# Kernel tuning notes

Measured on AMD Instinct MI355X. Metric: run time of the kernel, lower is better.

Reference implementation:

```python
import jax, jax.numpy as jnp
import numpy as np

H = 128  # hidden size
IN = 12  # input size
OUT = 4  # output classes


def _lstm_scan(gates_x, Whh, B, dtype, collect_ys):
    """gates_x: [T,B,4H] precomputed input-to-hidden gates (with biases).
    PyTorch gate order: i, f, g, o."""
    h0 = jnp.zeros((B, H), dtype)
    c0 = jnp.zeros((B, H), dtype)

    def step(carry, gx):
        h, c = carry
        g = gx + h @ Whh.T  # [B,4H]
        i, f, gg, o = jnp.split(g, 4, axis=-1)
        c = jax.nn.sigmoid(f) * c + jax.nn.sigmoid(i) * jnp.tanh(gg)
        h = jax.nn.sigmoid(o) * jnp.tanh(c)
        return (h, c), (h if collect_ys else None)

    (hT, cT), hs = jax.lax.scan(step, (h0, c0), gates_x)
    return hs, hT


def setup_inputs() -> dict:
    key = jax.random.key(0)
    ks = jax.random.split(key, 12)
    B, T = 256, 2048
    s = 1.0 / np.sqrt(H)  # torch LSTM/Linear init scale
    u = lambda k, shape: jax.random.uniform(k, shape, jnp.float32, -s, s)
    return {
        "x": jax.random.normal(ks[0], (B, T, IN), jnp.float32),
        "W_ih_l0": u(ks[1], (4 * H, IN)),
        "W_hh_l0": u(ks[2], (4 * H, H)),
        "b_ih_l0": u(ks[3], (4 * H,)),
        "b_hh_l0": u(ks[4], (4 * H,)),
        "W_ih_l1": u(ks[5], (4 * H, H)),
        "W_hh_l1": u(ks[6], (4 * H, H)),
        "b_ih_l1": u(ks[7], (4 * H,)),
        "b_hh_l1": u(ks[8], (4 * H,)),
        "W_out": u(ks[9], (OUT, H)),
        "b_out": u(ks[10], (OUT,)),
    }


def reference(x, W_ih_l0, W_hh_l0, b_ih_l0, b_hh_l0,
              W_ih_l1, W_hh_l1, b_ih_l1, b_hh_l1, W_out, b_out):
    B = x.shape[0]
    # layer 0: precompute all input projections at once -> [T,B,4H]
    gx0 = jnp.einsum('bti,gi->tbg', x, W_ih_l0) + b_ih_l0 + b_hh_l0
    hs0, _ = _lstm_scan(gx0, W_hh_l0, B, x.dtype, collect_ys=True)  # [T,B,H]
    # layer 1: only final hidden state is needed (r_out[:, -1] == h_T)
    gx1 = jnp.einsum('tbh,gh->tbg', hs0, W_ih_l1) + b_ih_l1 + b_hh_l1
    _, hT = _lstm_scan(gx1, W_hh_l1, B, x.dtype, collect_ys=False)  # [B,H]
    return hT @ W_out.T + b_out  # [B,4]
```

## Files before the change

### kernel.cpp

```cpp
#include <hip/hip_runtime.h>
#include <cstdint>
#include <cstddef>

#define H      128
#define IN_    12
#define GATES  512
#define B_     256
#define T_     2048
#define TCMAX  512
#define TT     64
#define PS     520

#define REP32(M) M(0) M(1) M(2) M(3) M(4) M(5) M(6) M(7) M(8) M(9) M(10) M(11) \
  M(12) M(13) M(14) M(15) M(16) M(17) M(18) M(19) M(20) M(21) M(22) M(23) \
  M(24) M(25) M(26) M(27) M(28) M(29) M(30) M(31)

__device__ __forceinline__ float sigmoidf_(float x) {
    return 1.f / (1.f + __expf(-x));
}
__device__ __forceinline__ float tanhf_(float x) {
    return 2.f / (1.f + __expf(-2.f * x)) - 1.f;
}
__device__ __forceinline__ float dot4f(float4 w, float4 h, float a) {
    return fmaf(w.x, h.x, fmaf(w.y, h.y, fmaf(w.z, h.z, fmaf(w.w, h.w, a))));
}

template<bool IS_L0>
__global__ __launch_bounds__(1024) void lstm_scan(
    const float* __restrict__ x_or_gx,
    const float* __restrict__ Wih,
    const float* __restrict__ Whh,
    const float* __restrict__ bih, const float* __restrict__ bhh,
    float* __restrict__ hs0,
    float* __restrict__ state,
    int tc, int chunk)
{
    const int b   = blockIdx.x;
    const int tid = threadIdx.x;
    const int ks  = tid >> 7;
    const int q   = tid & 127;

    extern __shared__ float smem[];
    float* sh_part = smem;
    float* sh_h    = smem + 8 * PS;
    float* sh_x    = sh_h + H;

#define LOADW(i) \
    const float4* wr##i = (const float4*)(Whh + (size_t)(4*q+i)*H + 16*ks); \
    float4 w##i##0 = wr##i[0], w##i##1 = wr##i[1], w##i##2 = wr##i[2], w##i##3 = wr##i[3];
    LOADW(0) LOADW(1) LOADW(2) LOADW(3)
#undef LOADW

    float4 wx0 = {0,0,0,0}, wx1 = {0,0,0,0}, wx2 = {0,0,0,0}, wx3 = {0,0,0,0};
    if constexpr (IS_L0) {
        if (ks >= 1 && ks <= 3) {
            wx0 = *(const float4*)(Wih + (size_t)(4*q+0)*IN_ + 4*(ks-1));
            wx1 = *(const float4*)(Wih + (size_t)(4*q+1)*IN_ + 4*(ks-1));
            wx2 = *(const float4*)(Wih + (size_t)(4*q+2)*IN_ + 4*(ks-1));
            wx3 = *(const float4*)(Wih + (size_t)(4*q+3)*IN_ + 4*(ks-1));
        }
        const float* xs = x_or_gx + ((size_t)b * T_ + (size_t)chunk * tc) * IN_;
        for (int i = tid; i < tc * IN_; i += 1024) sh_x[i] = xs[i];
    }

    float bias0 = 0, bias1 = 0, bias2 = 0, bias3 = 0;
    float cur0 = 0, cur1 = 0, cur2 = 0, cur3 = 0;
    float hreg = 0.f, creg = 0.f;
    const float* gxb = nullptr;
    if constexpr (!IS_L0) gxb = x_or_gx + (size_t)b * tc * GATES;

    if (tid < H) {
        if constexpr (IS_L0) {
            bias0 = bih[tid]       + bhh[tid];
            bias1 = bih[tid + 128] + bhh[tid + 128];
            bias2 = bih[tid + 256] + bhh[tid + 256];
            bias3 = bih[tid + 384] + bhh[tid + 384];
        } else {
            cur0 = gxb[tid]; cur1 = gxb[tid + 128];
            cur2 = gxb[tid + 256]; cur3 = gxb[tid + 384];
        }
        if (chunk) { hreg = state[b*2*H + tid]; creg = state[b*2*H + H + tid]; }
        sh_h[tid] = hreg;
    }
    __syncthreads();

    float* hs_out = nullptr;
    if constexpr (IS_L0) hs_out = hs0 + (size_t)b * tc * H;

    const float4* sh4 = (const float4*)sh_h;
    const int i0 = tid & 3, q0 = tid >> 2;

    for (int t = 0; t < tc; ++t) {
        float n0 = 0, n1 = 0, n2 = 0, n3 = 0;
        if constexpr (!IS_L0) {
            if (tid < H) {
                int tn = (t + 1 < tc) ? t + 1 : t;
                const float* gp = gxb + (size_t)tn * GATES;
                n0 = gp[tid]; n1 = gp[tid + 128];
                n2 = gp[tid + 256]; n3 = gp[tid + 384];
            }
        }
        float4 hA = sh4[4*ks], hB = sh4[4*ks+1], hC = sh4[4*ks+2], hD = sh4[4*ks+3];
        float a0 = dot4f(w03,hD, dot4f(w02,hC, dot4f(w01,hB, dot4f(w00,hA, 0.f))));
        float a1 = dot4f(w13,hD, dot4f(w12,hC, dot4f(w11,hB, dot4f(w10,hA, 0.f))));
        float a2 = dot4f(w23,hD, dot4f(w22,hC, dot4f(w21,hB, dot4f(w20,hA, 0.f))));
        float a3 = dot4f(w33,hD, dot4f(w32,hC, dot4f(w31,hB, dot4f(w30,hA, 0.f))));
        if constexpr (IS_L0) {
            if (ks >= 1 && ks <= 3) {
                float4 xq = *(const float4*)(sh_x + t * IN_ + 4*(ks-1));
                a0 = dot4f(wx0, xq, a0); a1 = dot4f(wx1, xq, a1);
                a2 = dot4f(wx2, xq, a2); a3 = dot4f(wx3, xq, a3);
            }
        }
        sh_part[ks*PS + 0*128 + q] = a0;
        sh_part[ks*PS + 1*128 + q] = a1;
        sh_part[ks*PS + 2*128 + q] = a2;
        sh_part[ks*PS + 3*128 + q] = a3;
        __syncthreads();

        if (tid < H) {
            float p0, p1, p2, p3;
            {
                const float* pb = sh_part + i0*128 + q0;
#define RSUM(m, dst) { \
                float s = pb[32*m]; \
                s += pb[32*m + 1*PS]; s += pb[32*m + 2*PS]; s += pb[32*m + 3*PS]; \
                s += pb[32*m + 4*PS]; s += pb[32*m + 5*PS]; s += pb[32*m + 6*PS]; \
                s += pb[32*m + 7*PS]; dst = s; }
                RSUM(0, p0) RSUM(1, p1) RSUM(2, p2) RSUM(3, p3)
#undef RSUM
            }
            float gi, gf, gg, go;
            if constexpr (IS_L0) {
                gi = p0 + bias0; gf = p1 + bias1; gg = p2 + bias2; go = p3 + bias3;
            } else {
                gi = p0 + cur0; gf = p1 + cur1; gg = p2 + cur2; go = p3 + cur3;
                cur0 = n0; cur1 = n1; cur2 = n2; cur3 = n3;
            }
            creg = fmaf(sigmoidf_(gf), creg, sigmoidf_(gi) * tanhf_(gg));
            hreg = sigmoidf_(go) * tanhf_(creg);
            sh_h[tid] = hreg;
            if constexpr (IS_L0) hs_out[(size_t)t * H + tid] = hreg;
        }
        __syncthreads();
    }
    if (tid < H) { state[b*2*H + tid] = hreg; state[b*2*H + H + tid] = creg; }
}

typedef __attribute__((ext_vector_type(16))) float f16x;

__global__ __launch_bounds__(512)
void gx1_gemm(const float* __restrict__ hs0, const float* __restrict__ Wih,
              const float* __restrict__ bih, const float* __restrict__ bhh,
              float* __restrict__ gx, int tc)
{
    const int b  = blockIdx.x;
    const int t0 = blockIdx.y * TT;
    const int g  = threadIdx.x;

#define LWG(j) float4 w##j = ((const float4*)(Wih + (size_t)g * H))[j];
    REP32(LWG)
#undef LWG
    const float biasg = bih[g] + bhh[g];

    const float* hp = hs0 + ((size_t)b * tc + t0) * H;
    float* gxo = gx + ((size_t)b * tc + t0) * GATES + g;

    for (int t = 0; t < TT; ++t) {
        const float* hpt = hp + (size_t)t * H;
        float a0 = biasg, a1 = 0.f, a2 = 0.f, a3 = 0.f;

        f16x h0, h1, h2, h3;
        asm volatile(
            "s_load_dwordx16 %0, %4, 0x0\n\t"
            "s_load_dwordx16 %1, %4, 0x40\n\t"
            "s_load_dwordx16 %2, %4, 0x80\n\t"
            "s_load_dwordx16 %3, %4, 0xc0\n\t"
            "s_waitcnt lgkmcnt(0)"
            : "=s"(h0), "=s"(h1), "=s"(h2), "=s"(h3)
            : "s"(hpt));
#define FMA16(hv, base) { \
        a0 = fmaf(w##base.x, hv.s0, a0);  a1 = fmaf(w##base.y, hv.s1, a1); \
        a2 = fmaf(w##base.z, hv.s2, a2);  a3 = fmaf(w##base.w, hv.s3, a3); }
#define Q4(hv, j0, j1, j2, j3) { \
        a0 = fmaf(w##j0.x, hv.s0, a0); a1 = fmaf(w##j0.y, hv.s1, a1); \
        a2 = fmaf(w##j0.z, hv.s2, a2); a3 = fmaf(w##j0.w, hv.s3, a3); \
        a0 = fmaf(w##j1.x, hv.s4, a0); a1 = fmaf(w##j1.y, hv.s5, a1); \
        a2 = fmaf(w##j1.z, hv.s6, a2); a3 = fmaf(w##j1.w, hv.s7, a3); \
        a0 = fmaf(w##j2.x, hv.s8, a0); a1 = fmaf(w##j2.y, hv.s9, a1); \
        a2 = fmaf(w##j2.z, hv.sa, a2); a3 = fmaf(w##j2.w, hv.sb, a3); \
        a0 = fmaf(w##j3.x, hv.sc, a0); a1 = fmaf(w##j3.y, hv.sd, a1); \
        a2 = fmaf(w##j3.z, hv.se, a2); a3 = fmaf(w##j3.w, hv.sf, a3); }
        Q4(h0, 0, 1, 2, 3)    Q4(h1, 4, 5, 6, 7)
        Q4(h2, 8, 9, 10, 11)  Q4(h3, 12, 13, 14, 15)

        asm volatile(
            "s_load_dwordx16 %0, %4, 0x100\n\t"
            "s_load_dwordx16 %1, %4, 0x140\n\t"
            "s_load_dwordx16 %2, %4, 0x180\n\t"
            "s_load_dwordx16 %3, %4, 0x1c0\n\t"
            "s_waitcnt lgkmcnt(0)"
            : "=s"(h0), "=s"(h1), "=s"(h2), "=s"(h3)
            : "s"(hpt));
        Q4(h0, 16, 17, 18, 19)  Q4(h1, 20, 21, 22, 23)
        Q4(h2, 24, 25, 26, 27)  Q4(h3, 28, 29, 30, 31)
#undef Q4
#undef FMA16

        gxo[(size_t)t * GATES] = (a0 + a1) + (a2 + a3);
    }
}

__global__ void out_proj(const float* __restrict__ state1,
                         const float* __restrict__ Wout,
                         const float* __restrict__ bout,
                         float* __restrict__ out)
{
    const int b = blockIdx.x, j = threadIdx.x;
    __shared__ float sh[H];
    if (j < H) sh[j] = state1[b*2*H + j];
    __syncthreads();
    if (j < 4) {
        float a = bout[j];
        for (int k = 0; k < H; ++k) a = fmaf(Wout[j*H + k], sh[k], a);
        out[b*4 + j] = a;
    }
}

extern "C" void kernel_launch(void* const* d_in, const int* in_sizes, int n_in,
                              void* d_out, int out_size, void* d_ws, size_t ws_size,
                              hipStream_t stream)
{
    const float* x    = (const float*)d_in[0];
    const float* Wih0 = (const float*)d_in[1];
    const float* Whh0 = (const float*)d_in[2];
    const float* bih0 = (const float*)d_in[3];
    const float* bhh0 = (const float*)d_in[4];
    const float* Wih1 = (const float*)d_in[5];
    const float* Whh1 = (const float*)d_in[6];
    const float* bih1 = (const float*)d_in[7];
    const float* bhh1 = (const float*)d_in[8];
    const float* Wout = (const float*)d_in[9];
    const float* bout = (const float*)d_in[10];

    int tc = TT;
    for (int cand = TCMAX; cand >= TT; cand >>= 1) {
        size_t need = (size_t)2 * B_ * 2 * H * 4
                    + (size_t)B_ * cand * H * 4
                    + (size_t)B_ * cand * GATES * 4;
        if (need <= ws_size) { tc = cand; break; }
    }

    float* ws  = (float*)d_ws;
    float* st0 = ws;
    float* st1 = st0 + (size_t)B_ * 2 * H;
    float* hs0 = st1 + (size_t)B_ * 2 * H;
    float* gx1 = hs0 + (size_t)B_ * tc * H;

    const size_t shm_l0 = (size_t)(8 * PS + H + tc * IN_) * 4;
    const size_t shm_l1 = (size_t)(8 * PS + H) * 4;

    const int nchunks = T_ / tc;
    for (int c = 0; c < nchunks; ++c) {
        lstm_scan<true><<<B_, 1024, shm_l0, stream>>>(
            x, Wih0, Whh0, bih0, bhh0, hs0, st0, tc, c);
        gx1_gemm<<<dim3(B_, tc / TT), 512, 0, stream>>>(
            hs0, Wih1, bih1, bhh1, gx1, tc);
        lstm_scan<false><<<B_, 1024, shm_l1, stream>>>(
            gx1, nullptr, Whh1, nullptr, nullptr, nullptr, st1, tc, c);
    }
    out_proj<<<B_, 128, 0, stream>>>(st1, Wout, bout, (float*)d_out);
}
```

Baseline: 5.653 ms.

## Overlap layer-0 chunk with layer-1 previous chunk in a combined scan launch

Splits the scan kernel into a shared device body plus separate layer-0, layer-1 and paired kernels. The host loop now runs layer 0 on chunk c and layer 1 on chunk c-1 in one 512-block launch, with a prologue and an epilogue around it, so the two recurrences can run concurrently instead of back to back. The gain depends on whether two 1024-thread blocks can be resident on one CU; if registers limit residency to one block per CU, the 512 blocks run in two waves and little is gained. It also drops an unused macro.

```diff
diff --git a/kernel.cpp b/kernel.cpp
--- a/kernel.cpp
+++ b/kernel.cpp
@@ -26,21 +26,16 @@
 }
 
 template<bool IS_L0>
-__global__ __launch_bounds__(1024) void lstm_scan(
-    const float* __restrict__ x_or_gx,
-    const float* __restrict__ Wih,
-    const float* __restrict__ Whh,
-    const float* __restrict__ bih, const float* __restrict__ bhh,
-    float* __restrict__ hs0,
-    float* __restrict__ state,
-    int tc, int chunk)
-{
-    const int b   = blockIdx.x;
+__device__ __forceinline__ void scan_body(
+    int b, const float* __restrict__ x_or_gx, const float* __restrict__ Wih,
+    const float* __restrict__ Whh, const float* __restrict__ bih,
+    const float* __restrict__ bhh, float* __restrict__ hs0,
+    float* __restrict__ state, int tc, int chunk, float* smem)
+{
     const int tid = threadIdx.x;
     const int ks  = tid >> 7;
     const int q   = tid & 127;
 
-    extern __shared__ float smem[];
     float* sh_part = smem;
     float* sh_h    = smem + 8 * PS;
     float* sh_x    = sh_h + H;
@@ -147,6 +142,43 @@
     if (tid < H) { state[b*2*H + tid] = hreg; state[b*2*H + H + tid] = creg; }
 }
 
+__global__ __launch_bounds__(1024) void lstm_scan_l0(
+    const float* __restrict__ x, const float* __restrict__ Wih,
+    const float* __restrict__ Whh, const float* __restrict__ bih,
+    const float* __restrict__ bhh, float* __restrict__ hs0,
+    float* __restrict__ state, int tc, int chunk)
+{
+    extern __shared__ float smem[];
+    scan_body<true>(blockIdx.x, x, Wih, Whh, bih, bhh, hs0, state, tc, chunk, smem);
+}
+
+__global__ __launch_bounds__(1024) void lstm_scan_l1(
+    const float* __restrict__ gx, const float* __restrict__ Whh,
+    float* __restrict__ state, int tc, int chunk)
+{
+    extern __shared__ float smem[];
+    scan_body<false>(blockIdx.x, gx, nullptr, Whh, nullptr, nullptr,
+                     nullptr, state, tc, chunk, smem);
+}
+
+__global__ __launch_bounds__(1024) void lstm_pair(
+    const float* __restrict__ x, const float* __restrict__ Wih0,
+    const float* __restrict__ Whh0, const float* __restrict__ bih0,
+    const float* __restrict__ bhh0, float* __restrict__ hs0,
+    float* __restrict__ st0, int c0,
+    const float* __restrict__ gx1, const float* __restrict__ Whh1,
+    float* __restrict__ st1, int c1, int tc)
+{
+    extern __shared__ float smem[];
+    if (blockIdx.x < B_) {
+        scan_body<true>(blockIdx.x, x, Wih0, Whh0, bih0, bhh0, hs0, st0,
+                        tc, c0, smem);
+    } else {
+        scan_body<false>(blockIdx.x - B_, gx1, nullptr, Whh1, nullptr, nullptr,
+                         nullptr, st1, tc, c1, smem);
+    }
+}
+
 typedef __attribute__((ext_vector_type(16))) float f16x;
 
 __global__ __launch_bounds__(512)
@@ -179,9 +211,6 @@
             "s_waitcnt lgkmcnt(0)"
             : "=s"(h0), "=s"(h1), "=s"(h2), "=s"(h3)
             : "s"(hpt));
-#define FMA16(hv, base) { \
-        a0 = fmaf(w##base.x, hv.s0, a0);  a1 = fmaf(w##base.y, hv.s1, a1); \
-        a2 = fmaf(w##base.z, hv.s2, a2);  a3 = fmaf(w##base.w, hv.s3, a3); }
 #define Q4(hv, j0, j1, j2, j3) { \
         a0 = fmaf(w##j0.x, hv.s0, a0); a1 = fmaf(w##j0.y, hv.s1, a1); \
         a2 = fmaf(w##j0.z, hv.s2, a2); a3 = fmaf(w##j0.w, hv.s3, a3); \
@@ -205,7 +234,6 @@
         Q4(h0, 16, 17, 18, 19)  Q4(h1, 20, 21, 22, 23)
         Q4(h2, 24, 25, 26, 27)  Q4(h3, 28, 29, 30, 31)
 #undef Q4
-#undef FMA16
 
         gxo[(size_t)t * GATES] = (a0 + a1) + (a2 + a3);
     }
@@ -261,13 +289,18 @@
     const size_t shm_l1 = (size_t)(8 * PS + H) * 4;
 
     const int nchunks = T_ / tc;
-    for (int c = 0; c < nchunks; ++c) {
-        lstm_scan<true><<<B_, 1024, shm_l0, stream>>>(
-            x, Wih0, Whh0, bih0, bhh0, hs0, st0, tc, c);
+
+    lstm_scan_l0<<<B_, 1024, shm_l0, stream>>>(
+        x, Wih0, Whh0, bih0, bhh0, hs0, st0, tc, 0);
+    gx1_gemm<<<dim3(B_, tc / TT), 512, 0, stream>>>(
+        hs0, Wih1, bih1, bhh1, gx1, tc);
+    for (int c = 1; c < nchunks; ++c) {
+        lstm_pair<<<2 * B_, 1024, shm_l0, stream>>>(
+            x, Wih0, Whh0, bih0, bhh0, hs0, st0, c,
+            gx1, Whh1, st1, c - 1, tc);
         gx1_gemm<<<dim3(B_, tc / TT), 512, 0, stream>>>(
             hs0, Wih1, bih1, bhh1, gx1, tc);
-        lstm_scan<false><<<B_, 1024, shm_l1, stream>>>(
-            gx1, nullptr, Whh1, nullptr, nullptr, nullptr, st1, tc, c);
-    }
+    }
+    lstm_scan_l1<<<B_, 1024, shm_l1, stream>>>(gx1, Whh1, st1, tc, nchunks - 1);
     out_proj<<<B_, 128, 0, stream>>>(st1, Wout, bout, (float*)d_out);
 }
```

Result: no change. 5.655 ms (+0.0%).
